# Optimization experiments

Hardware: AMD Instinct MI355X
Metric: run time of the kernel (lower is better)

## Reference

```python
import jax, jax.numpy as jnp
import numpy as np

N = 50000       # nodes
E = 800000      # edges (before self-loops)
IN_DIM = 256
HID = 64
HEADS = 3
N_CLASSES = 40
NEG_SLOPE = 0.2  # PyG GATConv default negative_slope


def setup_inputs() -> dict:
    key = jax.random.key(0)
    ks = jax.random.split(key, 12)
    x = jax.random.normal(ks[0], (N, IN_DIM), jnp.float32)
    src = jax.random.randint(ks[1], (E,), 0, N, dtype=jnp.int32)
    off = jax.random.randint(ks[2], (E,), 1, N, dtype=jnp.int32)
    dst = (src + off) % N  # guarantees no self-loops
    edge_index = jnp.stack([src, dst], axis=0)
    g = 0.1
    W1 = jax.random.normal(ks[3], (IN_DIM, HEADS * HID), jnp.float32) * g
    att_src1 = jax.random.normal(ks[4], (HEADS, HID), jnp.float32) * g
    att_dst1 = jax.random.normal(ks[5], (HEADS, HID), jnp.float32) * g
    b1 = jnp.zeros((HEADS * HID,), jnp.float32)
    W2 = jax.random.normal(ks[6], (HEADS * HID, HEADS * HID), jnp.float32) * g
    att_src2 = jax.random.normal(ks[7], (HEADS, HID), jnp.float32) * g
    att_dst2 = jax.random.normal(ks[8], (HEADS, HID), jnp.float32) * g
    b2 = jnp.zeros((HEADS * HID,), jnp.float32)
    Wout = jax.random.normal(ks[9], (HEADS * HID, N_CLASSES), jnp.float32) * g
    bout = jnp.zeros((N_CLASSES,), jnp.float32)
    return {"x": x, "edge_index": edge_index,
            "W1": W1, "att_src1": att_src1, "att_dst1": att_dst1, "b1": b1,
            "W2": W2, "att_src2": att_src2, "att_dst2": att_dst2, "b2": b2,
            "Wout": Wout, "bout": bout}


def _segment_softmax(logits, seg, num_segments):
    # logits: [E', H], seg: [E'] destination node ids
    m = jax.ops.segment_max(logits, seg, num_segments=num_segments)
    e = jnp.exp(logits - m[seg])
    s = jax.ops.segment_sum(e, seg, num_segments=num_segments)
    return e / s[seg]


def _gat_layer(x, src, dst, W, att_src, att_dst, bias):
    n = x.shape[0]
    h = (x @ W).reshape(n, HEADS, HID)               # lin_src == lin_dst (x is a Tensor)
    a_src = jnp.sum(h * att_src, axis=-1)            # [N, H]
    a_dst = jnp.sum(h * att_dst, axis=-1)            # [N, H]
    alpha = jax.nn.leaky_relu(a_src[src] + a_dst[dst], NEG_SLOPE)  # [E', H]
    alpha = _segment_softmax(alpha, dst, n)
    msg = h[src] * alpha[:, :, None]                 # [E', H, C]
    out = jax.ops.segment_sum(msg, dst, num_segments=n)  # scatter-add aggregate
    return out.reshape(n, HEADS * HID) + bias        # concat heads + bias


def reference(x, edge_index, W1, att_src1, att_dst1, b1,
              W2, att_src2, att_dst2, b2, Wout, bout):
    n = x.shape[0]
    loop = jnp.arange(n, dtype=edge_index.dtype)
    src = jnp.concatenate([edge_index[0], loop])     # add_self_loops=True
    dst = jnp.concatenate([edge_index[1], loop])
    h = _gat_layer(x, src, dst, W1, att_src1, att_dst1, b1)
    h = jax.nn.relu(h)                               # dropout p=0 -> identity
    h = _gat_layer(h, src, dst, W2, att_src2, att_dst2, b2)
    h = jax.nn.relu(h)
    return h @ Wout + bout                           # node-level readout + outlayer
```

## Files before the change

kernel.cpp:

```cpp
#include <hip/hip_runtime.h>
#include <math.h>

#define NN 50000
#define NE 800000
#define KIN 256
#define F 192
#define NH 3
#define NC 40
#define NBLK 49

typedef unsigned short u16;
typedef unsigned int   u32;
typedef __attribute__((ext_vector_type(8))) short bf16x8;
typedef __attribute__((ext_vector_type(4))) float f32x4;

static __device__ __forceinline__ u16 f2bf(float f){
  u32 u = __float_as_uint(f);
  u32 r = (u + 0x7fffu + ((u >> 16) & 1u)) >> 16;
  return (u16)r;
}

__global__ void count_kernel(const int* __restrict__ dst, int* __restrict__ cnt){
  int e = blockIdx.x*256 + threadIdx.x;
  if (e < NE) atomicAdd(&cnt[dst[e]], 1);
}

__global__ __launch_bounds__(256) void partial_kernel(const int* __restrict__ cnt, int* __restrict__ partials){
  __shared__ int red[256];
  const int t = threadIdx.x;
  const int base = blockIdx.x*1024 + t*4;
  int s = 0;
  if (base + 3 < NN){
    int4 v = *(const int4*)&cnt[base];
    s = v.x + v.y + v.z + v.w;
  } else if (base < NN){
    for (int i=base; i<NN; i++) s += cnt[i];
  }
  red[t] = s;
  __syncthreads();
  for (int off=128; off; off>>=1){
    if (t < off) red[t] += red[t+off];
    __syncthreads();
  }
  if (t==0) partials[blockIdx.x] = red[0];
}

__global__ __launch_bounds__(64) void scan_partials(const int* __restrict__ partials,
                                                    int* __restrict__ offsets, int* __restrict__ row_ptr){
  const int lane = threadIdx.x;
  int p = (lane < NBLK)? partials[lane] : 0;
  int inc = p;
  #pragma unroll
  for (int off=1; off<64; off<<=1){
    int v = __shfl_up(inc, off);
    if (lane >= off) inc += v;
  }
  if (lane < NBLK) offsets[lane] = inc - p;
  if (lane == NBLK-1) row_ptr[NN] = inc;
}

__global__ __launch_bounds__(256) void emit_kernel(int* __restrict__ cnt,
                                                   const int* __restrict__ offsets,
                                                   int* __restrict__ row_ptr){
  __shared__ int ts[256];
  const int t = threadIdx.x;
  const int base = blockIdx.x*1024 + t*4;
  int4 v = make_int4(0,0,0,0);
  if (base + 3 < NN) v = *(const int4*)&cnt[base];
  else if (base < NN){
    v.x = cnt[base];
    if (base+1 < NN) v.y = cnt[base+1];
    if (base+2 < NN) v.z = cnt[base+2];
  }
  int tot = v.x + v.y + v.z + v.w;
  ts[t] = tot;
  __syncthreads();
  #pragma unroll
  for (int off=1; off<256; off<<=1){
    int val = (t >= off)? ts[t-off] : 0;
    __syncthreads();
    ts[t] += val;
    __syncthreads();
  }
  int off0 = offsets[blockIdx.x] + ts[t] - tot;
  if (base + 3 < NN){
    row_ptr[base]   = off0;
    row_ptr[base+1] = off0 + v.x;
    row_ptr[base+2] = off0 + v.x + v.y;
    row_ptr[base+3] = off0 + v.x + v.y + v.z;
    *(int4*)&cnt[base] = make_int4(0,0,0,0);
  } else if (base < NN){
    row_ptr[base] = off0; cnt[base] = 0;
    if (base+1 < NN){ row_ptr[base+1] = off0 + v.x; cnt[base+1] = 0; }
    if (base+2 < NN){ row_ptr[base+2] = off0 + v.x + v.y; cnt[base+2] = 0; }
  }
}

__global__ void fill_kernel(const int* __restrict__ src, const int* __restrict__ dst,
                            const int* __restrict__ row_ptr, int* __restrict__ cur,
                            int* __restrict__ col){
  int e = blockIdx.x*256 + threadIdx.x;
  if (e < NE){
    int d = dst[e];
    int p = row_ptr[d] + atomicAdd(&cur[d], 1);
    col[p] = src[e];
  }
}

__global__ void conv_all(const float* __restrict__ W1, const float* __restrict__ W2,
                         const float* __restrict__ Wout,
                         u16* __restrict__ w1t, u16* __restrict__ w2t, u16* __restrict__ wot){
  int e = blockIdx.x*256 + threadIdx.x;
  if (e < F*KIN){
    int c = e / KIN, r = e % KIN;
    w1t[e] = f2bf(W1[(size_t)r*F + c]);
    return;
  }
  int e2 = e - F*KIN;
  if (e2 < F*F){
    int c = e2 / F, r = e2 % F;
    w2t[e2] = f2bf(W2[(size_t)r*F + c]);
    return;
  }
  int e3 = e2 - F*F;
  if (e3 < 48*F){
    int n = e3 / F, k = e3 % F;
    wot[e3] = (n < NC)? f2bf(Wout[(size_t)k*NC + n]) : (u16)0;
  }
}

#define SAK 72
#define SC  196
template<int K, bool CONVA>
__global__ __launch_bounds__(256) void gemm_mfma(const void* __restrict__ Araw, const u16* __restrict__ Bt,
                                                 u16* __restrict__ C,
                                                 const float* __restrict__ att_src, const float* __restrict__ att_dst,
                                                 float* __restrict__ a_src4, float* __restrict__ a_dst4){
  __shared__ __align__(16) union {
    struct { u16 As[64*SAK]; u16 Bs[192*SAK]; } st;
    u16 Cs[64*SC];
  } sh;
  const int t = threadIdx.x;
  const int wave = t >> 6, lane = t & 63;
  const int quad = lane >> 4, l16 = lane & 15;
  const int r0 = blockIdx.x*64;

  f32x4 acc[4][3];
  #pragma unroll
  for (int rt=0;rt<4;rt++)
    #pragma unroll
    for (int ct=0;ct<3;ct++) acc[rt][ct] = (f32x4){0.f,0.f,0.f,0.f};

  for (int k0=0; k0<K; k0+=64){
    __syncthreads();
    {
      int row = t >> 2, kq = (t & 3)*16;
      bool ok = (r0+row) < NN;
      if (CONVA){
        const float* Af = (const float*)Araw;
        float4 v0 = make_float4(0,0,0,0), v1 = v0, v2 = v0, v3 = v0;
        if (ok){
          const float* p = &Af[(size_t)(r0+row)*K + k0 + kq];
          v0 = *(const float4*)(p+0);
          v1 = *(const float4*)(p+4);
          v2 = *(const float4*)(p+8);
          v3 = *(const float4*)(p+12);
        }
        uint4 pa, pb;
        pa.x = (u32)f2bf(v0.x) | ((u32)f2bf(v0.y) << 16);
        pa.y = (u32)f2bf(v0.z) | ((u32)f2bf(v0.w) << 16);
        pa.z = (u32)f2bf(v1.x) | ((u32)f2bf(v1.y) << 16);
        pa.w = (u32)f2bf(v1.z) | ((u32)f2bf(v1.w) << 16);
        pb.x = (u32)f2bf(v2.x) | ((u32)f2bf(v2.y) << 16);
        pb.y = (u32)f2bf(v2.z) | ((u32)f2bf(v2.w) << 16);
        pb.z = (u32)f2bf(v3.x) | ((u32)f2bf(v3.y) << 16);
        pb.w = (u32)f2bf(v3.z) | ((u32)f2bf(v3.w) << 16);
        *(uint4*)&sh.st.As[row*SAK + kq]     = pa;
        *(uint4*)&sh.st.As[row*SAK + kq + 8] = pb;
      } else {
        const u16* Ab = (const u16*)Araw;
        uint4 va = make_uint4(0,0,0,0), vb = va;
        if (ok){
          va = *(const uint4*)&Ab[(size_t)(r0+row)*K + k0 + kq];
          vb = *(const uint4*)&Ab[(size_t)(r0+row)*K + k0 + kq + 8];
        }
        *(uint4*)&sh.st.As[row*SAK + kq]     = va;
        *(uint4*)&sh.st.As[row*SAK + kq + 8] = vb;
      }
    }
    #pragma unroll
    for (int i=0;i<6;i++){
      int idx = t + i*256;
      int n = idx >> 3, kc = idx & 7;
      *(uint4*)&sh.st.Bs[n*SAK + kc*8] = *(const uint4*)&Bt[(size_t)n*K + k0 + kc*8];
    }
    __syncthreads();
    bf16x8 af[4][2], bf[3][2];
    #pragma unroll
    for (int kf=0;kf<2;kf++){
      #pragma unroll
      for (int rt=0;rt<4;rt++) af[rt][kf] = *(const bf16x8*)&sh.st.As[(rt*16 + l16)*SAK + kf*32 + quad*8];
      #pragma unroll
      for (int ct=0;ct<3;ct++) bf[ct][kf] = *(const bf16x8*)&sh.st.Bs[(wave*48 + ct*16 + l16)*SAK + kf*32 + quad*8];
    }
    #pragma unroll
    for (int kf=0;kf<2;kf++)
      #pragma unroll
      for (int rt=0;rt<4;rt++)
        #pragma unroll
        for (int ct=0;ct<3;ct++)
          acc[rt][ct] = __builtin_amdgcn_mfma_f32_16x16x32_bf16(af[rt][kf], bf[ct][kf], acc[rt][ct], 0, 0, 0);
  }

  __syncthreads();
  #pragma unroll
  for (int ct=0;ct<3;ct++){
    const int n = wave*48 + ct*16 + l16;
    #pragma unroll
    for (int rt=0;rt<4;rt++){
      #pragma unroll
      for (int reg=0;reg<4;reg++){
        const int m = rt*16 + quad*4 + reg;
        sh.Cs[m*SC + n] = f2bf(acc[rt][ct][reg]);
      }
    }
  }
  __syncthreads();
  {
    int row = t >> 2, c0 = (t & 3)*6;
    int grow = r0 + row;
    if (grow < NN){
      #pragma unroll
      for (int j=0;j<6;j++){
        int ch = c0 + j;
        uint4 v = *(const uint4*)&sh.Cs[row*SC + ch*8];
        *(uint4*)&C[(size_t)grow*F + ch*8] = v;
      }
    }
  }
  if (t < 192){
    int row = t & 63, head = t >> 6;
    int grow = r0 + row;
    if (grow < NN){
      float ps = 0.f, pd = 0.f;
      #pragma unroll
      for (int j=0;j<8;j++){
        uint4 v = *(const uint4*)&sh.Cs[row*SC + head*64 + j*8];
        float4 w0 = *(const float4*)&att_src[head*64 + j*8];
        float4 w1 = *(const float4*)&att_src[head*64 + j*8 + 4];
        float4 d0 = *(const float4*)&att_dst[head*64 + j*8];
        float4 d1 = *(const float4*)&att_dst[head*64 + j*8 + 4];
        float c0f = __uint_as_float(v.x << 16), c1f = __uint_as_float(v.x & 0xffff0000u);
        float c2f = __uint_as_float(v.y << 16), c3f = __uint_as_float(v.y & 0xffff0000u);
        float c4f = __uint_as_float(v.z << 16), c5f = __uint_as_float(v.z & 0xffff0000u);
        float c6f = __uint_as_float(v.w << 16), c7f = __uint_as_float(v.w & 0xffff0000u);
        ps = fmaf(c0f,w0.x,fmaf(c1f,w0.y,fmaf(c2f,w0.z,fmaf(c3f,w0.w,ps))));
        ps = fmaf(c4f,w1.x,fmaf(c5f,w1.y,fmaf(c6f,w1.z,fmaf(c7f,w1.w,ps))));
        pd = fmaf(c0f,d0.x,fmaf(c1f,d0.y,fmaf(c2f,d0.z,fmaf(c3f,d0.w,pd))));
        pd = fmaf(c4f,d1.x,fmaf(c5f,d1.y,fmaf(c6f,d1.z,fmaf(c7f,d1.w,pd))));
      }
      a_src4[(size_t)grow*4 + head] = ps;
      a_dst4[(size_t)grow*4 + head] = pd;
    }
  }
}

__global__ __launch_bounds__(256) void gat_agg_wave(const u16* __restrict__ hb,
    const float* __restrict__ a_src4, const float* __restrict__ a_dst4,
    const int* __restrict__ row_ptr, const int* __restrict__ col,
    const float* __restrict__ bias, u16* __restrict__ out){
  __shared__ float s_al[4][64][4];
  const int t = threadIdx.x;
  const int lane = t & 63;
  const int w = t >> 6;
  const int d = blockIdx.x*4 + w;
  if (d >= NN) return;
  const int e0  = row_ptr[d];
  const int deg = row_ptr[d+1] - e0;
  const int ecount = deg + 1;
  const float4 ad = *(const float4*)&a_dst4[(size_t)d*4];

  float s0=0.f, s1=0.f, s2=0.f;
  int   sn_r = d;
  float e0r=0.f, e1r=0.f, e2r=0.f;
  const int lastBase = ((ecount-1) >> 6) << 6;

  for (int base=0; base<ecount; base+=64){
    int j = base + lane;
    bool valid = j < ecount;
    int sn = d;
    if (j < deg) sn = col[e0+j];
    float4 as = *(const float4*)&a_src4[(size_t)sn*4];
    float l0 = as.x + ad.x; l0 = (l0>0.f)? l0 : 0.2f*l0;
    float l1 = as.y + ad.y; l1 = (l1>0.f)? l1 : 0.2f*l1;
    float l2 = as.z + ad.z; l2 = (l2>0.f)? l2 : 0.2f*l2;
    float E0 = valid? __expf(l0) : 0.f;
    float E1 = valid? __expf(l1) : 0.f;
    float E2 = valid? __expf(l2) : 0.f;
    float S0=E0, S1=E1, S2=E2;
    #pragma unroll
    for (int off=32; off; off>>=1){
      S0 += __shfl_xor(S0, off);
      S1 += __shfl_xor(S1, off);
      S2 += __shfl_xor(S2, off);
    }
    s0 += S0; s1 += S1; s2 += S2;
    sn_r = sn; e0r = E0; e1r = E1; e2r = E2;
  }
  const float i0 = 1.f/s0, i1 = 1.f/s1, i2 = 1.f/s2;

  const int cg = (lane < 48)? lane : lane - 48;
  const int hg = (lane < 48)? (lane >> 4) : (lane >> 4) - 3;
  const int cgo = cg*4;
  float4 acc = make_float4(0.f,0.f,0.f,0.f);
  for (int base=0; base<ecount; base+=64){
    int sn; float E0,E1,E2;
    if (base == lastBase){ sn = sn_r; E0 = e0r; E1 = e1r; E2 = e2r; }
    else {
      int j = base + lane;
      sn = (j < deg)? col[e0+j] : d;
      float4 as = *(const float4*)&a_src4[(size_t)sn*4];
      float l0 = as.x + ad.x; l0 = (l0>0.f)? l0 : 0.2f*l0;
      float l1 = as.y + ad.y; l1 = (l1>0.f)? l1 : 0.2f*l1;
      float l2 = as.z + ad.z; l2 = (l2>0.f)? l2 : 0.2f*l2;
      E0 = __expf(l0); E1 = __expf(l1); E2 = __expf(l2);
    }
    float4 st;
    st.x = E0*i0; st.y = E1*i1; st.z = E2*i2; st.w = 0.f;
    *(float4*)&s_al[w][lane][0] = st;
    __builtin_amdgcn_wave_barrier();
    int cnt = ecount - base; if (cnt > 64) cnt = 64;
    int jj = 0;
    for (; jj+4 <= cnt; jj += 4){
      int sA = __builtin_amdgcn_readlane(sn, jj);
      int sB = __builtin_amdgcn_readlane(sn, jj+1);
      int sC = __builtin_amdgcn_readlane(sn, jj+2);
      int sD = __builtin_amdgcn_readlane(sn, jj+3);
      uint2 pA = *(const uint2*)(hb + sA*F + cgo);
      uint2 pB = *(const uint2*)(hb + sB*F + cgo);
      uint2 pC = *(const uint2*)(hb + sC*F + cgo);
      uint2 pD = *(const uint2*)(hb + sD*F + cgo);
      float aA = s_al[w][jj  ][hg];
      float aB = s_al[w][jj+1][hg];
      float aC = s_al[w][jj+2][hg];
      float aD = s_al[w][jj+3][hg];
      acc.x = fmaf(aA, __uint_as_float(pA.x << 16),         acc.x);
      acc.y = fmaf(aA, __uint_as_float(pA.x & 0xffff0000u), acc.y);
      acc.z = fmaf(aA, __uint_as_float(pA.y << 16),         acc.z);
      acc.w = fmaf(aA, __uint_as_float(pA.y & 0xffff0000u), acc.w);
      acc.x = fmaf(aB, __uint_as_float(pB.x << 16),         acc.x);
      acc.y = fmaf(aB, __uint_as_float(pB.x & 0xffff0000u), acc.y);
      acc.z = fmaf(aB, __uint_as_float(pB.y << 16),         acc.z);
      acc.w = fmaf(aB, __uint_as_float(pB.y & 0xffff0000u), acc.w);
      acc.x = fmaf(aC, __uint_as_float(pC.x << 16),         acc.x);
      acc.y = fmaf(aC, __uint_as_float(pC.x & 0xffff0000u), acc.y);
      acc.z = fmaf(aC, __uint_as_float(pC.y << 16),         acc.z);
      acc.w = fmaf(aC, __uint_as_float(pC.y & 0xffff0000u), acc.w);
      acc.x = fmaf(aD, __uint_as_float(pD.x << 16),         acc.x);
      acc.y = fmaf(aD, __uint_as_float(pD.x & 0xffff0000u), acc.y);
      acc.z = fmaf(aD, __uint_as_float(pD.y << 16),         acc.z);
      acc.w = fmaf(aD, __uint_as_float(pD.y & 0xffff0000u), acc.w);
    }
    for (; jj < cnt; jj++){
      int sA = __builtin_amdgcn_readlane(sn, jj);
      uint2 pA = *(const uint2*)(hb + sA*F + cgo);
      float aA = s_al[w][jj][hg];
      acc.x = fmaf(aA, __uint_as_float(pA.x << 16),         acc.x);
      acc.y = fmaf(aA, __uint_as_float(pA.x & 0xffff0000u), acc.y);
      acc.z = fmaf(aA, __uint_as_float(pA.y << 16),         acc.z);
      acc.w = fmaf(aA, __uint_as_float(pA.y & 0xffff0000u), acc.w);
    }
    __builtin_amdgcn_wave_barrier();
  }
  if (lane < 48){
    float4 b4 = *(const float4*)&bias[cg*4];
    uint2 o;
    o.x = (u32)f2bf(fmaxf(acc.x + b4.x, 0.f)) | ((u32)f2bf(fmaxf(acc.y + b4.y, 0.f)) << 16);
    o.y = (u32)f2bf(fmaxf(acc.z + b4.z, 0.f)) | ((u32)f2bf(fmaxf(acc.w + b4.w, 0.f)) << 16);
    *(uint2*)&out[(size_t)d*F + cg*4] = o;
  }
}

__global__ __launch_bounds__(256) void gemm_out_mfma(const u16* __restrict__ A,
    const u16* __restrict__ Wt, const float* __restrict__ bias, float* __restrict__ out){
  const int t = threadIdx.x;
  const int wave = t >> 6, lane = t & 63;
  const int quad = lane >> 4, l16 = lane & 15;
  const int rbase = blockIdx.x*64 + wave*16;
  const int arow = rbase + l16;
  f32x4 acc[3];
  #pragma unroll
  for (int ct=0;ct<3;ct++) acc[ct] = (f32x4){0.f,0.f,0.f,0.f};
  #pragma unroll
  for (int ks=0; ks<6; ks++){
    const int k0 = ks*32;
    union { uint4 u; bf16x8 h; } cva;
    cva.u = make_uint4(0,0,0,0);
    if (arow < NN) cva.u = *(const uint4*)&A[(size_t)arow*F + k0 + quad*8];
    #pragma unroll
    for (int ct=0;ct<3;ct++){
      bf16x8 bfr = *(const bf16x8*)&Wt[(size_t)(ct*16 + l16)*F + k0 + quad*8];
      acc[ct] = __builtin_amdgcn_mfma_f32_16x16x32_bf16(cva.h, bfr, acc[ct], 0, 0, 0);
    }
  }
  #pragma unroll
  for (int ct=0;ct<3;ct++){
    const int n = ct*16 + l16;
    #pragma unroll
    for (int reg=0;reg<4;reg++){
      const int m = quad*4 + reg;
      const int grow = rbase + m;
      if (grow < NN && n < NC) out[(size_t)grow*NC + n] = acc[ct][reg] + bias[n];
    }
  }
}

extern "C" void kernel_launch(void* const* d_in, const int* in_sizes, int n_in,
                              void* d_out, int out_size, void* d_ws, size_t ws_size,
                              hipStream_t stream){
  const float* x    = (const float*)d_in[0];
  const int*   ei   = (const int*)  d_in[1];
  const float* W1   = (const float*)d_in[2];
  const float* as1  = (const float*)d_in[3];
  const float* ad1  = (const float*)d_in[4];
  const float* b1   = (const float*)d_in[5];
  const float* W2   = (const float*)d_in[6];
  const float* as2  = (const float*)d_in[7];
  const float* ad2  = (const float*)d_in[8];
  const float* b2   = (const float*)d_in[9];
  const float* Wout = (const float*)d_in[10];
  const float* bout = (const float*)d_in[11];
  float* out = (float*)d_out;

  u16* w1t = (u16*)d_ws;
  u16* w2t = w1t + (size_t)F*KIN;
  u16* wot = w2t + (size_t)F*F;
  u16* hb1 = wot + (size_t)48*F;
  u16* hb2 = hb1 + (size_t)NN*F;
  u16* gb1 = hb2 + (size_t)NN*F;
  u16* gb2 = gb1 + (size_t)NN*F;
  float* a_src4 = (float*)(gb2 + (size_t)NN*F);
  float* a_dst4 = a_src4 + (size_t)NN*4;
  int* row_ptr  = (int*)(a_dst4 + (size_t)NN*4);
  int* col      = row_ptr + (NN+1);
  int* cnt      = col + NE;
  int* partials = cnt + NN;
  int* offsets  = partials + NBLK;

  const int* srcv = ei;
  const int* dstv = ei + NE;

  hipMemsetAsync(cnt, 0, NN*sizeof(int), stream);
  count_kernel<<<(NE+255)/256, 256, 0, stream>>>(dstv, cnt);
  partial_kernel<<<NBLK, 256, 0, stream>>>(cnt, partials);
  scan_partials<<<1, 64, 0, stream>>>(partials, offsets, row_ptr);
  emit_kernel<<<NBLK, 256, 0, stream>>>(cnt, offsets, row_ptr);
  fill_kernel<<<(NE+255)/256, 256, 0, stream>>>(srcv, dstv, row_ptr, cnt, col);

  const int CONV_N = F*KIN + F*F + 48*F;
  conv_all<<<(CONV_N + 255)/256, 256, 0, stream>>>(W1, W2, Wout, w1t, w2t, wot);

  const int GEMM_GRID = (NN + 63)/64;
  const int AGG_GRID  = (NN + 3)/4;
  gemm_mfma<KIN,true><<<GEMM_GRID, 256, 0, stream>>>(x, w1t, hb1, as1, ad1, a_src4, a_dst4);
  gat_agg_wave<<<AGG_GRID, 256, 0, stream>>>(hb1, a_src4, a_dst4, row_ptr, col, b1, gb1);
  gemm_mfma<F,false><<<GEMM_GRID, 256, 0, stream>>>(gb1, w2t, hb2, as2, ad2, a_src4, a_dst4);
  gat_agg_wave<<<AGG_GRID, 256, 0, stream>>>(hb2, a_src4, a_dst4, row_ptr, col, b2, gb2);
  gemm_out_mfma<<<GEMM_GRID, 256, 0, stream>>>(gb2, wot, bout, out);
}
```

Measured before the change: 346.1 us.

## Single-pass GAT aggregation with deferred softmax normalization; merge weight conversion into count kernel

The aggregation kernel now gathers features once per edge chunk using unnormalized exp weights. It accumulates the per-head sums per lane, reduces them with one shuffle tree at the end, and applies 1/sum with a fused multiply-add before bias and relu. This removes the separate first pass over col and a_src4 and the per-chunk shuffle reductions. Separately, the weight transpose/bf16 conversion is folded into the edge-count kernel as extra blocks, saving one kernel launch. The risk is that skipping max-subtraction can overflow exp for large logits, as the original also did.

```diff
diff --git a/kernel.cpp b/kernel.cpp
--- a/kernel.cpp
+++ b/kernel.cpp
@@ -8,6 +8,9 @@
 #define NH 3
 #define NC 40
 #define NBLK 49
+#define CNT_BLKS ((NE+255)/256)
+#define CONV_N (F*KIN + F*F + 48*F)
+#define CONV_BLKS ((CONV_N+255)/256)
 
 typedef unsigned short u16;
 typedef unsigned int   u32;
@@ -20,9 +23,33 @@
   return (u16)r;
 }
 
-__global__ void count_kernel(const int* __restrict__ dst, int* __restrict__ cnt){
-  int e = blockIdx.x*256 + threadIdx.x;
-  if (e < NE) atomicAdd(&cnt[dst[e]], 1);
+__global__ void count_conv_kernel(const int* __restrict__ dst, int* __restrict__ cnt,
+                                  const float* __restrict__ W1, const float* __restrict__ W2,
+                                  const float* __restrict__ Wout,
+                                  u16* __restrict__ w1t, u16* __restrict__ w2t, u16* __restrict__ wot){
+  int b = blockIdx.x;
+  if (b < CNT_BLKS){
+    int e = b*256 + threadIdx.x;
+    if (e < NE) atomicAdd(&cnt[dst[e]], 1);
+    return;
+  }
+  int e = (b - CNT_BLKS)*256 + threadIdx.x;
+  if (e < F*KIN){
+    int c = e / KIN, r = e % KIN;
+    w1t[e] = f2bf(W1[(size_t)r*F + c]);
+    return;
+  }
+  int e2 = e - F*KIN;
+  if (e2 < F*F){
+    int c = e2 / F, r = e2 % F;
+    w2t[e2] = f2bf(W2[(size_t)r*F + c]);
+    return;
+  }
+  int e3 = e2 - F*F;
+  if (e3 < 48*F){
+    int n = e3 / F, k = e3 % F;
+    wot[e3] = (n < NC)? f2bf(Wout[(size_t)k*NC + n]) : (u16)0;
+  }
 }
 
 __global__ __launch_bounds__(256) void partial_kernel(const int* __restrict__ cnt, int* __restrict__ partials){
@@ -104,28 +131,6 @@
     int d = dst[e];
     int p = row_ptr[d] + atomicAdd(&cur[d], 1);
     col[p] = src[e];
-  }
-}
-
-__global__ void conv_all(const float* __restrict__ W1, const float* __restrict__ W2,
-                         const float* __restrict__ Wout,
-                         u16* __restrict__ w1t, u16* __restrict__ w2t, u16* __restrict__ wot){
-  int e = blockIdx.x*256 + threadIdx.x;
-  if (e < F*KIN){
-    int c = e / KIN, r = e % KIN;
-    w1t[e] = f2bf(W1[(size_t)r*F + c]);
-    return;
-  }
-  int e2 = e - F*KIN;
-  if (e2 < F*F){
-    int c = e2 / F, r = e2 % F;
-    w2t[e2] = f2bf(W2[(size_t)r*F + c]);
-    return;
-  }
-  int e3 = e2 - F*F;
-  if (e3 < 48*F){
-    int n = e3 / F, k = e3 % F;
-    wot[e3] = (n < NC)? f2bf(Wout[(size_t)k*NC + n]) : (u16)0;
   }
 }
 
@@ -280,10 +285,11 @@
   const int ecount = deg + 1;
   const float4 ad = *(const float4*)&a_dst4[(size_t)d*4];
 
-  float s0=0.f, s1=0.f, s2=0.f;
-  int   sn_r = d;
-  float e0r=0.f, e1r=0.f, e2r=0.f;
-  const int lastBase = ((ecount-1) >> 6) << 6;
+  const int cg = (lane < 48)? lane : lane - 48;
+  const int hg = (lane < 48)? (lane >> 4) : 0;
+  const int cgo = cg*4;
+  float4 acc = make_float4(0.f,0.f,0.f,0.f);
+  float sl0=0.f, sl1=0.f, sl2=0.f;
 
   for (int base=0; base<ecount; base+=64){
     int j = base + lane;
@@ -297,36 +303,8 @@
     float E0 = valid? __expf(l0) : 0.f;
     float E1 = valid? __expf(l1) : 0.f;
     float E2 = valid? __expf(l2) : 0.f;
-    float S0=E0, S1=E1, S2=E2;
-    #pragma unroll
-    for (int off=32; off; off>>=1){
-      S0 += __shfl_xor(S0, off);
-      S1 += __shfl_xor(S1, off);
-      S2 += __shfl_xor(S2, off);
-    }
-    s0 += S0; s1 += S1; s2 += S2;
-    sn_r = sn; e0r = E0; e1r = E1; e2r = E2;
-  }
-  const float i0 = 1.f/s0, i1 = 1.f/s1, i2 = 1.f/s2;
-
-  const int cg = (lane < 48)? lane : lane - 48;
-  const int hg = (lane < 48)? (lane >> 4) : (lane >> 4) - 3;
-  const int cgo = cg*4;
-  float4 acc = make_float4(0.f,0.f,0.f,0.f);
-  for (int base=0; base<ecount; base+=64){
-    int sn; float E0,E1,E2;
-    if (base == lastBase){ sn = sn_r; E0 = e0r; E1 = e1r; E2 = e2r; }
-    else {
-      int j = base + lane;
-      sn = (j < deg)? col[e0+j] : d;
-      float4 as = *(const float4*)&a_src4[(size_t)sn*4];
-      float l0 = as.x + ad.x; l0 = (l0>0.f)? l0 : 0.2f*l0;
-      float l1 = as.y + ad.y; l1 = (l1>0.f)? l1 : 0.2f*l1;
-      float l2 = as.z + ad.z; l2 = (l2>0.f)? l2 : 0.2f*l2;
-      E0 = __expf(l0); E1 = __expf(l1); E2 = __expf(l2);
-    }
-    float4 st;
-    st.x = E0*i0; st.y = E1*i1; st.z = E2*i2; st.w = 0.f;
+    sl0 += E0; sl1 += E1; sl2 += E2;
+    float4 st; st.x = E0; st.y = E1; st.z = E2; st.w = 0.f;
     *(float4*)&s_al[w][lane][0] = st;
     __builtin_amdgcn_wave_barrier();
     int cnt = ecount - base; if (cnt > 64) cnt = 64;
@@ -372,11 +350,20 @@
     }
     __builtin_amdgcn_wave_barrier();
   }
+  #pragma unroll
+  for (int off=32; off; off>>=1){
+    sl0 += __shfl_xor(sl0, off);
+    sl1 += __shfl_xor(sl1, off);
+    sl2 += __shfl_xor(sl2, off);
+  }
   if (lane < 48){
+    float inv = 1.f / ((hg==0)? sl0 : ((hg==1)? sl1 : sl2));
     float4 b4 = *(const float4*)&bias[cg*4];
     uint2 o;
-    o.x = (u32)f2bf(fmaxf(acc.x + b4.x, 0.f)) | ((u32)f2bf(fmaxf(acc.y + b4.y, 0.f)) << 16);
-    o.y = (u32)f2bf(fmaxf(acc.z + b4.z, 0.f)) | ((u32)f2bf(fmaxf(acc.w + b4.w, 0.f)) << 16);
+    o.x = (u32)f2bf(fmaxf(fmaf(acc.x, inv, b4.x), 0.f))
+        | ((u32)f2bf(fmaxf(fmaf(acc.y, inv, b4.y), 0.f)) << 16);
+    o.y = (u32)f2bf(fmaxf(fmaf(acc.z, inv, b4.z), 0.f))
+        | ((u32)f2bf(fmaxf(fmaf(acc.w, inv, b4.w), 0.f)) << 16);
     *(uint2*)&out[(size_t)d*F + cg*4] = o;
   }
 }
@@ -451,14 +438,11 @@
   const int* dstv = ei + NE;
 
   hipMemsetAsync(cnt, 0, NN*sizeof(int), stream);
-  count_kernel<<<(NE+255)/256, 256, 0, stream>>>(dstv, cnt);
+  count_conv_kernel<<<CNT_BLKS + CONV_BLKS, 256, 0, stream>>>(dstv, cnt, W1, W2, Wout, w1t, w2t, wot);
   partial_kernel<<<NBLK, 256, 0, stream>>>(cnt, partials);
   scan_partials<<<1, 64, 0, stream>>>(partials, offsets, row_ptr);
   emit_kernel<<<NBLK, 256, 0, stream>>>(cnt, offsets, row_ptr);
   fill_kernel<<<(NE+255)/256, 256, 0, stream>>>(srcv, dstv, row_ptr, cnt, col);
-
-  const int CONV_N = F*KIN + F*F + 48*F;
-  conv_all<<<(CONV_N + 255)/256, 256, 0, stream>>>(W1, W2, Wout, w1t, w2t, wot);
 
   const int GEMM_GRID = (NN + 63)/64;
   const int AGG_GRID  = (NN + 3)/4;
```

After: 343.5 us (median of 2 runs). No clear change (-0.8%).
